# Performance work log

Hardware: AMD Instinct MI355X
Metric: run time of the kernel (lower is better)

Reference implementation:

```python
import jax, jax.numpy as jnp
import numpy as np

N_NODES = 50000


def _gcn_layer(x, edge_index, W, b, relu):
    """tf_geometric-style GCN: h = D^-1/2 (A+I) D^-1/2 (x @ W) + b, opt relu."""
    n = x.shape[0]
    h = x @ W  # [N, D_out] transform first (standard GCN)
    src, dst = edge_index[0], edge_index[1]
    sl = jnp.arange(n, dtype=src.dtype)
    src = jnp.concatenate([src, sl])  # add self-loops (renorm trick)
    dst = jnp.concatenate([dst, sl])
    deg = jax.ops.segment_sum(jnp.ones_like(dst, dtype=h.dtype), dst, num_segments=n)
    dinv = jax.lax.rsqrt(jnp.maximum(deg, 1e-12))
    norm = dinv[src] * dinv[dst]  # symmetric normalization per edge
    msg = h[src] * norm[:, None]  # [E+N, D_out] gather + scale
    out = jax.ops.segment_sum(msg, dst, num_segments=n) + b
    return jax.nn.relu(out) if relu else out


def setup_inputs() -> dict:
    key = jax.random.key(0)
    ks = jax.random.split(key, 12)
    F, E = 512, 800000
    d = {}
    d["x"] = jax.random.normal(ks[0], (N_NODES, F), dtype=jnp.float32)
    d["edge_index1"] = jax.random.randint(ks[1], (2, E), 0, N_NODES, dtype=jnp.int32)
    d["edge_index2"] = jax.random.randint(ks[2], (2, E), 0, N_NODES, dtype=jnp.int32)
    def glorot(k, shape):
        lim = np.sqrt(6.0 / (shape[0] + shape[1])).astype(np.float32)
        return jax.random.uniform(k, shape, jnp.float32, -lim, lim)
    d["W10"] = glorot(ks[3], (F, 256)); d["b10"] = jnp.zeros((256,), jnp.float32)
    d["W20"] = glorot(ks[4], (F, 64));  d["b20"] = jnp.zeros((64,), jnp.float32)
    d["W21"] = glorot(ks[5], (64, 256)); d["b21"] = jnp.zeros((256,), jnp.float32)
    d["Wfc"] = glorot(ks[6], (256, 16)); d["bfc"] = jnp.zeros((16,), jnp.float32)
    return d


def reference(x, edge_index1, edge_index2, W10, b10, W20, b20, W21, b21, Wfc, bfc):
    h1 = _gcn_layer(x, edge_index1, W10, b10, relu=True)   # GCN(256, relu)
    h2 = _gcn_layer(x, edge_index2, W20, b20, relu=False)  # GCN(64)
    h2 = _gcn_layer(h2, edge_index2, W21, b21, relu=True)  # GCN(256, relu)
    h = h1 + h2
    return h @ Wfc + bfc  # Dense(class_num)
```

## Files before the change

### kernel.cpp

```cpp
#include <hip/hip_runtime.h>
#include <hip/hip_bf16.h>
#include <cstdint>
#include <cstddef>

#define N_NODES 50000
#define FDIM 512
#define NBKT 391
#define CHUNK 8192
#define BCAP 4096

typedef __bf16 bf16_t;
typedef bf16_t bf16x8 __attribute__((ext_vector_type(8)));
typedef float f32x4 __attribute__((ext_vector_type(4)));

__device__ __forceinline__ unsigned short f2bf(float f) {
  union { float f; uint32_t u; } c; c.f = f;
  uint32_t u = c.u;
  uint32_t r = (u + 0x7fffu + ((u >> 16) & 1u)) >> 16;
  return (unsigned short)r;
}
__device__ __forceinline__ float bf2f(unsigned short u) {
  union { uint32_t i; float f; } c; c.i = (uint32_t)u << 16; return c.f;
}
__device__ __forceinline__ float4 ld_bf4(const unsigned short* p) {
  ushort4 u = *(const ushort4*)p;
  float4 r; r.x = bf2f(u.x); r.y = bf2f(u.y); r.z = bf2f(u.z); r.w = bf2f(u.w);
  return r;
}
__device__ __forceinline__ void async16(const void* g, void* l) {
  __builtin_amdgcn_global_load_lds((const __attribute__((address_space(1))) void*)g,
                                   (__attribute__((address_space(3))) void*)l, 16, 0, 0);
}

__global__ __launch_bounds__(256) void binA(const int* __restrict__ d1, const int* __restrict__ d2,
                                            int* __restrict__ M1, int* __restrict__ M2,
                                            int E1, int E2, int nch1, int nch2) {
  const int g = blockIdx.y;
  const int* dst = g ? d2 : d1;
  int* M = g ? M2 : M1;
  const int E = g ? E2 : E1;
  const int nch = g ? nch2 : nch1;
  const int chunk = blockIdx.x;
  if (chunk >= nch) return;
  __shared__ int cnt[NBKT];
  for (int j = threadIdx.x; j < NBKT; j += 256) cnt[j] = 0;
  __syncthreads();
  const int base = chunk * CHUNK;
#pragma unroll 4
  for (int i = 0; i < CHUNK / 256; i++) {
    int e = base + i * 256 + threadIdx.x;
    if (e < E) atomicAdd(&cnt[dst[e] >> 7], 1);
  }
  __syncthreads();
  for (int j = threadIdx.x; j < NBKT; j += 256) M[chunk * NBKT + j] = cnt[j];
}

__global__ __launch_bounds__(512) void bin_offsets(int* __restrict__ M1, int* __restrict__ M2,
                                                   int* __restrict__ bases,
                                                   int nch1, int nch2, int E1, int E2) {
  const int g = blockIdx.x;
  int* M = g ? M2 : M1;
  const int nch = g ? nch2 : nch1;
  int* base = bases + g * (NBKT + 1);
  const int E = g ? E2 : E1;
  const int t = threadIdx.x;
  __shared__ int tot[512];
  int running = 0;
  if (t < NBKT) {
    for (int b = 0; b < nch; b++) {
      int v = M[b * NBKT + t];
      M[b * NBKT + t] = running;
      running += v;
    }
  }
  tot[t] = (t < NBKT) ? running : 0;
  __syncthreads();
  for (int off = 1; off < 512; off <<= 1) {
    int u = (t >= off) ? tot[t - off] : 0;
    __syncthreads();
    tot[t] += u;
    __syncthreads();
  }
  int ex = (t == 0) ? 0 : tot[t - 1];
  if (t < NBKT) {
    base[t] = ex;
    for (int b = 0; b < nch; b++) M[b * NBKT + t] += ex;
  }
  if (t == NBKT) base[NBKT] = E;
}

__global__ __launch_bounds__(256) void binB(const int* __restrict__ s1, const int* __restrict__ d1,
                                            const int* __restrict__ M1, unsigned* __restrict__ eb1,
                                            int E1, int nch1,
                                            const int* __restrict__ s2, const int* __restrict__ d2,
                                            const int* __restrict__ M2, unsigned* __restrict__ eb2,
                                            int E2, int nch2) {
  const int g = blockIdx.y;
  const int* src = g ? s2 : s1;
  const int* dst = g ? d2 : d1;
  const int* M = g ? M2 : M1;
  unsigned* eb = g ? eb2 : eb1;
  const int E = g ? E2 : E1;
  const int nch = g ? nch2 : nch1;
  const int chunk = blockIdx.x;
  if (chunk >= nch) return;
  __shared__ int gbase[NBKT];
  __shared__ int cur[NBKT];
  for (int j = threadIdx.x; j < NBKT; j += 256) {
    gbase[j] = M[chunk * NBKT + j];
    cur[j] = 0;
  }
  __syncthreads();
  const int base = chunk * CHUNK;
#pragma unroll 4
  for (int i = 0; i < CHUNK / 256; i++) {
    int e = base + i * 256 + threadIdx.x;
    if (e < E) {
      int d = dst[e];
      int b = d >> 7;
      int pos = gbase[b] + atomicAdd(&cur[b], 1);
      eb[pos] = ((unsigned)d << 16) | (unsigned)src[e];
    }
  }
}

__global__ __launch_bounds__(256) void binC(const unsigned* __restrict__ eb1,
                                            const unsigned* __restrict__ eb2,
                                            const int* __restrict__ bases,
                                            int* __restrict__ rp1, float* __restrict__ dv1,
                                            int* __restrict__ cs1,
                                            int* __restrict__ rp2, float* __restrict__ dv2,
                                            int* __restrict__ cs2, int n) {
  const int g = blockIdx.y;
  const unsigned* eb = g ? eb2 : eb1;
  const int* base = bases + g * (NBKT + 1);
  int* rp = g ? rp2 : rp1;
  float* dv = g ? dv2 : dv1;
  int* cs = g ? cs2 : cs1;
  const int bkt = blockIdx.x;
  const int e0 = base[bkt], e1 = base[bkt + 1];
  const int cnt = e1 - e0;
  const int node0 = bkt << 7;
  const int t = threadIdx.x;
  __shared__ unsigned stage[BCAP];
  __shared__ int sorted[BCAP];
  __shared__ int dcnt[128], dcur[128], dscan[128];
  if (t < 128) dcnt[t] = 0;
  __syncthreads();
  for (int i = t; i < cnt; i += 256) {
    unsigned pe = eb[e0 + i];
    stage[i] = pe;
    atomicAdd(&dcnt[(pe >> 16) & 127], 1);
  }
  __syncthreads();
  if (t < 128) dscan[t] = dcnt[t];
  __syncthreads();
  for (int off = 1; off < 128; off <<= 1) {
    int u = (t < 128 && t >= off) ? dscan[t - off] : 0;
    __syncthreads();
    if (t < 128) dscan[t] += u;
    __syncthreads();
  }
  if (t < 128) {
    int ex = dscan[t] - dcnt[t];
    dcur[t] = ex;
    int node = node0 + t;
    if (node < n) {
      rp[node] = e0 + ex;
      dv[node] = rsqrtf((float)dcnt[t] + 1.0f);
    }
  }
  __syncthreads();
  for (int i = t; i < cnt; i += 256) {
    unsigned pe = stage[i];
    int d = (pe >> 16) & 127;
    int pos = atomicAdd(&dcur[d], 1);
    sorted[pos] = (int)(pe & 0xFFFFu);
  }
  __syncthreads();
  for (int i = t; i < cnt; i += 256) cs[e0 + i] = sorted[i];
  if (bkt == NBKT - 1 && t == 0) rp[n] = base[NBKT];
}

__global__ void cvt_w(const float* __restrict__ W10, const float* __restrict__ W20,
                      const float* __restrict__ W21, unsigned short* __restrict__ WcatT,
                      unsigned short* __restrict__ W21T) {
  int j = blockIdx.x * 256 + threadIdx.x;
  const int T1 = 384 * 512;
  if (j < T1) {
    int n = j >> 9, k = j & 511;
    float v = (n < 256) ? W10[k * 256 + n] : ((n < 320) ? W20[k * 64 + (n - 256)] : 0.f);
    WcatT[j] = f2bf(v);
  } else {
    int j2 = j - T1;
    if (j2 < 256 * 64) {
      int n = j2 >> 6, k = j2 & 63;
      W21T[j2] = f2bf(W21[k * 256 + n]);
    }
  }
}

__global__ __launch_bounds__(256) void g1(const float* __restrict__ X,
                                          const unsigned short* __restrict__ B,
                                          unsigned short* __restrict__ o1,
                                          unsigned short* __restrict__ o2, int M) {
  __shared__ __attribute__((aligned(16))) unsigned short As[128 * 64];
  __shared__ __attribute__((aligned(16))) unsigned short Bs[128 * 64];
  const int tid = threadIdx.x;
  const int w = tid >> 6, lane = tid & 63;
  const int row0 = blockIdx.x * 128;
  const int n0 = blockIdx.y * 128;
  const int lr = lane >> 3, lc8 = (lane & 7) * 8;
  const int wm = w >> 1, wn = w & 1;
  const int mlane = lane & 15, q = lane >> 4;

  f32x4 acc[4][4];
#pragma unroll
  for (int mi = 0; mi < 4; mi++)
#pragma unroll
    for (int ni = 0; ni < 4; ni++) {
      f32x4 z = {0.f, 0.f, 0.f, 0.f};
      acc[mi][ni] = z;
    }

  for (int k0 = 0; k0 < 512; k0 += 64) {
    __syncthreads();
#pragma unroll
    for (int i = 0; i < 8; i++) {
      int j = i * 256 + tid;
      int r = j >> 4, c4 = j & 15;
      int gr = row0 + r; if (gr > M - 1) gr = M - 1;
      float4 v = *(const float4*)(X + (size_t)gr * 512 + k0 + c4 * 4);
      ushort4 o; o.x = f2bf(v.x); o.y = f2bf(v.y); o.z = f2bf(v.z); o.w = f2bf(v.w);
      *(ushort4*)&As[r * 64 + c4 * 4] = o;
    }
#pragma unroll
    for (int i = 0; i < 4; i++) {
      int n = i * 32 + w * 8 + lr;
      async16(B + (size_t)(n0 + n) * 512 + k0 + lc8, &Bs[(i * 32 + w * 8) * 64]);
    }
    __syncthreads();
#pragma unroll
    for (int kk = 0; kk < 2; kk++) {
      bf16x8 af[4], bfr[4];
#pragma unroll
      for (int mi = 0; mi < 4; mi++)
        af[mi] = *(const bf16x8*)&As[(wm * 64 + mi * 16 + mlane) * 64 + kk * 32 + q * 8];
#pragma unroll
      for (int ni = 0; ni < 4; ni++)
        bfr[ni] = *(const bf16x8*)&Bs[(wn * 64 + ni * 16 + mlane) * 64 + kk * 32 + q * 8];
#pragma unroll
      for (int mi = 0; mi < 4; mi++)
#pragma unroll
        for (int ni = 0; ni < 4; ni++)
          acc[mi][ni] = __builtin_amdgcn_mfma_f32_16x16x32_bf16(af[mi], bfr[ni], acc[mi][ni], 0, 0, 0);
    }
  }

#pragma unroll
  for (int mi = 0; mi < 4; mi++)
#pragma unroll
    for (int ni = 0; ni < 4; ni++) {
      int c = n0 + wn * 64 + ni * 16 + mlane;
#pragma unroll
      for (int rg = 0; rg < 4; rg++) {
        int r = row0 + wm * 64 + mi * 16 + q * 4 + rg;
        if (r < M) {
          float v = acc[mi][ni][rg];
          if (c < 256) o1[(size_t)r * 256 + c] = f2bf(v);
          else if (c < 320) o2[(size_t)r * 64 + (c - 256)] = f2bf(v);
        }
      }
    }
}

__global__ __launch_bounds__(256) void prop256(const unsigned short* __restrict__ H,
                                               const int* __restrict__ rp,
                                               const int* __restrict__ cs,
                                               const float* __restrict__ dinv,
                                               const float* __restrict__ bias,
                                               float* __restrict__ out, int n) {
  const int i = blockIdx.x * 4 + (threadIdx.x >> 6);
  const int l = threadIdx.x & 63;
  if (i >= n) return;
  const float di = dinv[i];
  float4 self = ld_bf4(H + (size_t)i * 256 + l * 4);
  float4 acc;
  acc.x = di * self.x; acc.y = di * self.y; acc.z = di * self.z; acc.w = di * self.w;
  const int e1 = rp[i + 1];
#pragma unroll 4
  for (int e = rp[i]; e < e1; e++) {
    int s = cs[e];
    float wgt = dinv[s];
    float4 rrow = ld_bf4(H + (size_t)s * 256 + l * 4);
    acc.x += wgt * rrow.x; acc.y += wgt * rrow.y; acc.z += wgt * rrow.z; acc.w += wgt * rrow.w;
  }
  float4 b = *(const float4*)(bias + l * 4);
  float4 o;
  o.x = fmaxf(di * acc.x + b.x, 0.f);
  o.y = fmaxf(di * acc.y + b.y, 0.f);
  o.z = fmaxf(di * acc.z + b.z, 0.f);
  o.w = fmaxf(di * acc.w + b.w, 0.f);
  *(float4*)(out + (size_t)i * 256 + l * 4) = o;
}

template <int BIAS>
__global__ __launch_bounds__(256) void prop64(const unsigned short* __restrict__ H,
                                              const int* __restrict__ rp,
                                              const int* __restrict__ cs,
                                              const float* __restrict__ dinv,
                                              const float* __restrict__ bias,
                                              unsigned short* __restrict__ out, int n) {
  const int i = blockIdx.x * 16 + (threadIdx.x >> 4);
  const int l = threadIdx.x & 15;
  if (i >= n) return;
  const float di = dinv[i];
  float4 self = ld_bf4(H + (size_t)i * 64 + l * 4);
  float4 acc;
  acc.x = di * self.x; acc.y = di * self.y; acc.z = di * self.z; acc.w = di * self.w;
  const int e1 = rp[i + 1];
#pragma unroll 4
  for (int e = rp[i]; e < e1; e++) {
    int s = cs[e];
    float wgt = dinv[s];
    float4 rrow = ld_bf4(H + (size_t)s * 64 + l * 4);
    acc.x += wgt * rrow.x; acc.y += wgt * rrow.y; acc.z += wgt * rrow.z; acc.w += wgt * rrow.w;
  }
  float4 o;
  o.x = di * acc.x; o.y = di * acc.y; o.z = di * acc.z; o.w = di * acc.w;
  if (BIAS) {
    float4 b = *(const float4*)(bias + l * 4);
    o.x += b.x; o.y += b.y; o.z += b.z; o.w += b.w;
  }
  ushort4 ob;
  ob.x = f2bf(o.x); ob.y = f2bf(o.y); ob.z = f2bf(o.z); ob.w = f2bf(o.w);
  *(ushort4*)(out + (size_t)i * 64 + l * 4) = ob;
}

__global__ __launch_bounds__(512) void gf(const unsigned short* __restrict__ A,
                                          const unsigned short* __restrict__ Bb,
                                          const float* __restrict__ h1,
                                          const float* __restrict__ b21,
                                          const float* __restrict__ Wfc,
                                          const float* __restrict__ bfc,
                                          float* __restrict__ out, int M) {
  __shared__ __attribute__((aligned(16))) float hsm[128 * 260];
  __shared__ __attribute__((aligned(16))) float wt[256 * 16];
  unsigned short* As = (unsigned short*)hsm;
  unsigned short* Bs = As + 128 * 64;
  const int tid = threadIdx.x;
  const int w = tid >> 6, lane = tid & 63;
  const int row0 = blockIdx.x * 128;
  const int wm = w >> 2, wn = w & 3;
  const int mlane = lane & 15, q = lane >> 4;

  for (int j = tid; j < 4096; j += 512) wt[j] = Wfc[j];
#pragma unroll
  for (int i = 0; i < 2; i++) {
    int gr = row0 + i * 64 + w * 8 + (lane >> 3);
    if (gr > M - 1) gr = M - 1;
    async16(A + (size_t)gr * 64 + (lane & 7) * 8, &As[(i * 64 + w * 8) * 64]);
  }
#pragma unroll
  for (int i = 0; i < 4; i++) {
    int n = i * 64 + w * 8 + (lane >> 3);
    async16(Bb + (size_t)n * 64 + (lane & 7) * 8, &Bs[(i * 64 + w * 8) * 64]);
  }
  __syncthreads();

  f32x4 acc[4][4];
#pragma unroll
  for (int mi = 0; mi < 4; mi++)
#pragma unroll
    for (int ni = 0; ni < 4; ni++) {
      f32x4 z = {0.f, 0.f, 0.f, 0.f};
      acc[mi][ni] = z;
    }
#pragma unroll
  for (int kk = 0; kk < 2; kk++) {
    bf16x8 af[4], bfr[4];
#pragma unroll
    for (int mi = 0; mi < 4; mi++)
      af[mi] = *(const bf16x8*)&As[(wm * 64 + mi * 16 + mlane) * 64 + kk * 32 + q * 8];
#pragma unroll
    for (int ni = 0; ni < 4; ni++)
      bfr[ni] = *(const bf16x8*)&Bs[(wn * 64 + ni * 16 + mlane) * 64 + kk * 32 + q * 8];
#pragma unroll
    for (int mi = 0; mi < 4; mi++)
#pragma unroll
      for (int ni = 0; ni < 4; ni++)
        acc[mi][ni] = __builtin_amdgcn_mfma_f32_16x16x32_bf16(af[mi], bfr[ni], acc[mi][ni], 0, 0, 0);
  }
  __syncthreads();

#pragma unroll
  for (int ni = 0; ni < 4; ni++) {
    int c = wn * 64 + ni * 16 + mlane;
    float bb = b21[c];
#pragma unroll
    for (int mi = 0; mi < 4; mi++)
#pragma unroll
      for (int rg = 0; rg < 4; rg++) {
        int rl = wm * 64 + mi * 16 + q * 4 + rg;
        int gr = row0 + rl;
        int grc = (gr < M) ? gr : (M - 1);
        float v = fmaxf(acc[mi][ni][rg] + bb, 0.f) + h1[(size_t)grc * 256 + c];
        hsm[rl * 260 + c] = v;
      }
  }
  __syncthreads();

  const int r = tid >> 2, j0 = (tid & 3) * 4;
  const int gr = row0 + r;
  if (gr < M) {
    float4 s = *(const float4*)(bfc + j0);
    const float* hrow = &hsm[r * 260];
#pragma unroll 8
    for (int c4 = 0; c4 < 64; c4++) {
      float4 h4 = *(const float4*)(hrow + c4 * 4);
      const float* wp = &wt[(c4 * 4) * 16 + j0];
      float4 a0 = *(const float4*)(wp);
      float4 a1 = *(const float4*)(wp + 16);
      float4 a2 = *(const float4*)(wp + 32);
      float4 a3 = *(const float4*)(wp + 48);
      s.x += h4.x * a0.x + h4.y * a1.x + h4.z * a2.x + h4.w * a3.x;
      s.y += h4.x * a0.y + h4.y * a1.y + h4.z * a2.y + h4.w * a3.y;
      s.z += h4.x * a0.z + h4.y * a1.z + h4.z * a2.z + h4.w * a3.z;
      s.w += h4.x * a0.w + h4.y * a1.w + h4.z * a2.w + h4.w * a3.w;
    }
    *(float4*)(out + (size_t)gr * 16 + j0) = s;
  }
}

extern "C" void kernel_launch(void* const* d_in, const int* in_sizes, int n_in,
                              void* d_out, int out_size, void* d_ws, size_t ws_size,
                              hipStream_t stream) {
  const float* X   = (const float*)d_in[0];
  const int*   ei1 = (const int*)d_in[1];
  const int*   ei2 = (const int*)d_in[2];
  const float* W10 = (const float*)d_in[3];
  const float* b10 = (const float*)d_in[4];
  const float* W20 = (const float*)d_in[5];
  const float* b20 = (const float*)d_in[6];
  const float* W21 = (const float*)d_in[7];
  const float* b21 = (const float*)d_in[8];
  const float* Wfc = (const float*)d_in[9];
  const float* bfc = (const float*)d_in[10];
  float* out = (float*)d_out;

  const int N = N_NODES;
  const int E1 = in_sizes[1] / 2, E2 = in_sizes[2] / 2;
  const int* src1 = ei1; const int* dst1 = ei1 + E1;
  const int* src2 = ei2; const int* dst2 = ei2 + E2;
  const int nch1 = (E1 + CHUNK - 1) / CHUNK, nch2 = (E2 + CHUNK - 1) / CHUNK;
  const int nchmax = (nch1 > nch2) ? nch1 : nch2;

  char* p = (char*)d_ws;
  auto alloc = [&](size_t b) { char* r = p; p += (b + 255) & ~(size_t)255; return (void*)r; };
  int* M1 = (int*)alloc((size_t)nch1 * NBKT * 4);
  int* M2 = (int*)alloc((size_t)nch2 * NBKT * 4);
  int* bases = (int*)alloc((size_t)2 * (NBKT + 1) * 4);
  unsigned* eb1 = (unsigned*)alloc((size_t)E1 * 4);
  unsigned* eb2 = (unsigned*)alloc((size_t)E2 * 4);
  int* rp1 = (int*)alloc((size_t)(N + 1) * 4);
  int* rp2 = (int*)alloc((size_t)(N + 1) * 4);
  float* dinv1 = (float*)alloc((size_t)N * 4);
  float* dinv2 = (float*)alloc((size_t)N * 4);
  int* csr1s = (int*)alloc((size_t)E1 * 4);
  int* csr2s = (int*)alloc((size_t)E2 * 4);
  unsigned short* WcatT = (unsigned short*)alloc(384 * 512 * 2);
  unsigned short* W21T  = (unsigned short*)alloc(256 * 64 * 2);
  unsigned short* Xh1b = (unsigned short*)alloc((size_t)N * 256 * 2);
  unsigned short* Xh2b = (unsigned short*)alloc((size_t)N * 64 * 2);
  unsigned short* h2b  = (unsigned short*)alloc((size_t)N * 64 * 2);
  unsigned short* q2b  = (unsigned short*)alloc((size_t)N * 64 * 2);
  float* h1 = (float*)alloc((size_t)N * 256 * 4);

  binA<<<dim3(nchmax, 2), 256, 0, stream>>>(dst1, dst2, M1, M2, E1, E2, nch1, nch2);
  bin_offsets<<<dim3(2), 512, 0, stream>>>(M1, M2, bases, nch1, nch2, E1, E2);
  binB<<<dim3(nchmax, 2), 256, 0, stream>>>(src1, dst1, M1, eb1, E1, nch1,
                                            src2, dst2, M2, eb2, E2, nch2);
  binC<<<dim3(NBKT, 2), 256, 0, stream>>>(eb1, eb2, bases, rp1, dinv1, csr1s,
                                          rp2, dinv2, csr2s, N);
  cvt_w<<<dim3((384 * 512 + 256 * 64 + 255) / 256), 256, 0, stream>>>(W10, W20, W21, WcatT, W21T);
  g1<<<dim3((N + 127) / 128, 3), 256, 0, stream>>>(X, WcatT, Xh1b, Xh2b, N);
  prop256<<<dim3((N + 3) / 4), 256, 0, stream>>>(Xh1b, rp1, csr1s, dinv1, b10, h1, N);
  prop64<1><<<dim3((N + 15) / 16), 256, 0, stream>>>(Xh2b, rp2, csr2s, dinv2, b20, h2b, N);
  prop64<0><<<dim3((N + 15) / 16), 256, 0, stream>>>(h2b, rp2, csr2s, dinv2, nullptr, q2b, N);
  gf<<<dim3((N + 127) / 128), 512, 0, stream>>>(q2b, W21T, h1, b21, Wfc, bfc, out, N);
}
```

Measured before the change: 429.3 us.

## Widen first GEMM N-tile to 192 and prefetch X into registers across k-steps

The X@Wcat GEMM now uses 128x192 tiles with a grid of 2 column blocks instead of 3. The fp32 X matrix is therefore read twice rather than three times. The next k-slice of X is prefetched into registers while the current slice is converted and computed, with explicit waitcnt and barrier scheduling. This cuts redundant global reads of X and hides load latency, at the cost of more accumulator registers (24 MFMA tiles) and more LDS, which may lower occupancy. It also adds unroll pragmas to the bin offset loops.

Measured after the change: 430.7 us. Within noise of the previous version (+0.3%).

```diff
diff --git a/kernel.cpp b/kernel.cpp
--- a/kernel.cpp
+++ b/kernel.cpp
@@ -67,6 +67,7 @@
   __shared__ int tot[512];
   int running = 0;
   if (t < NBKT) {
+#pragma unroll 4
     for (int b = 0; b < nch; b++) {
       int v = M[b * NBKT + t];
       M[b * NBKT + t] = running;
@@ -84,6 +85,7 @@
   int ex = (t == 0) ? 0 : tot[t - 1];
   if (t < NBKT) {
     base[t] = ex;
+#pragma unroll 4
     for (int b = 0; b < nch; b++) M[b * NBKT + t] += ex;
   }
   if (t == NBKT) base[NBKT] = E;
@@ -200,59 +202,84 @@
   }
 }
 
-__global__ __launch_bounds__(256) void g1(const float* __restrict__ X,
-                                          const unsigned short* __restrict__ B,
-                                          unsigned short* __restrict__ o1,
-                                          unsigned short* __restrict__ o2, int M) {
+__global__ __launch_bounds__(256) void g1w(const float* __restrict__ X,
+                                           const unsigned short* __restrict__ B,
+                                           unsigned short* __restrict__ o1,
+                                           unsigned short* __restrict__ o2, int M) {
   __shared__ __attribute__((aligned(16))) unsigned short As[128 * 64];
-  __shared__ __attribute__((aligned(16))) unsigned short Bs[128 * 64];
+  __shared__ __attribute__((aligned(16))) unsigned short Bs[192 * 64];
   const int tid = threadIdx.x;
   const int w = tid >> 6, lane = tid & 63;
   const int row0 = blockIdx.x * 128;
-  const int n0 = blockIdx.y * 128;
-  const int lr = lane >> 3, lc8 = (lane & 7) * 8;
+  const int n0 = blockIdx.y * 192;
   const int wm = w >> 1, wn = w & 1;
   const int mlane = lane & 15, q = lane >> 4;
 
-  f32x4 acc[4][4];
+  const int ar = tid >> 4;
+  const int ac4 = tid & 15;
+
+  f32x4 acc[4][6];
 #pragma unroll
   for (int mi = 0; mi < 4; mi++)
 #pragma unroll
-    for (int ni = 0; ni < 4; ni++) {
+    for (int ni = 0; ni < 6; ni++) {
       f32x4 z = {0.f, 0.f, 0.f, 0.f};
       acc[mi][ni] = z;
     }
 
+  float4 areg[8];
+#pragma unroll
+  for (int i = 0; i < 8; i++) {
+    int gr = row0 + i * 16 + ar; if (gr > M - 1) gr = M - 1;
+    areg[i] = *(const float4*)(X + (size_t)gr * 512 + ac4 * 4);
+  }
+
   for (int k0 = 0; k0 < 512; k0 += 64) {
     __syncthreads();
 #pragma unroll
     for (int i = 0; i < 8; i++) {
-      int j = i * 256 + tid;
-      int r = j >> 4, c4 = j & 15;
-      int gr = row0 + r; if (gr > M - 1) gr = M - 1;
-      float4 v = *(const float4*)(X + (size_t)gr * 512 + k0 + c4 * 4);
-      ushort4 o; o.x = f2bf(v.x); o.y = f2bf(v.y); o.z = f2bf(v.z); o.w = f2bf(v.w);
-      *(ushort4*)&As[r * 64 + c4 * 4] = o;
-    }
-#pragma unroll
-    for (int i = 0; i < 4; i++) {
-      int n = i * 32 + w * 8 + lr;
-      async16(B + (size_t)(n0 + n) * 512 + k0 + lc8, &Bs[(i * 32 + w * 8) * 64]);
-    }
-    __syncthreads();
+      ushort4 o;
+      o.x = f2bf(areg[i].x); o.y = f2bf(areg[i].y);
+      o.z = f2bf(areg[i].z); o.w = f2bf(areg[i].w);
+      *(ushort4*)&As[(i * 16 + ar) * 64 + ac4 * 4] = o;
+    }
+#pragma unroll
+    for (int i = 0; i < 6; i++) {
+      int idx = i * 256 + tid;
+      int rw = idx >> 3, c8 = idx & 7;
+      async16(B + (size_t)(n0 + rw) * 512 + k0 + c8 * 8, &Bs[rw * 64 + c8 * 8]);
+    }
+    __builtin_amdgcn_sched_barrier(0);
+    const bool lastk = (k0 == 448);
+    if (!lastk) {
+#pragma unroll
+      for (int i = 0; i < 8; i++) {
+        int gr = row0 + i * 16 + ar; if (gr > M - 1) gr = M - 1;
+        areg[i] = *(const float4*)(X + (size_t)gr * 512 + (k0 + 64) + ac4 * 4);
+      }
+    }
+    __builtin_amdgcn_sched_barrier(0);
+    if (!lastk) {
+      asm volatile("s_waitcnt vmcnt(8) lgkmcnt(0)" ::: "memory");
+    } else {
+      asm volatile("s_waitcnt vmcnt(0) lgkmcnt(0)" ::: "memory");
+    }
+    __builtin_amdgcn_sched_barrier(0);
+    __builtin_amdgcn_s_barrier();
+    __builtin_amdgcn_sched_barrier(0);
 #pragma unroll
     for (int kk = 0; kk < 2; kk++) {
-      bf16x8 af[4], bfr[4];
+      bf16x8 af[4], bfr[6];
 #pragma unroll
       for (int mi = 0; mi < 4; mi++)
         af[mi] = *(const bf16x8*)&As[(wm * 64 + mi * 16 + mlane) * 64 + kk * 32 + q * 8];
 #pragma unroll
-      for (int ni = 0; ni < 4; ni++)
-        bfr[ni] = *(const bf16x8*)&Bs[(wn * 64 + ni * 16 + mlane) * 64 + kk * 32 + q * 8];
+      for (int ni = 0; ni < 6; ni++)
+        bfr[ni] = *(const bf16x8*)&Bs[(wn * 96 + ni * 16 + mlane) * 64 + kk * 32 + q * 8];
 #pragma unroll
       for (int mi = 0; mi < 4; mi++)
 #pragma unroll
-        for (int ni = 0; ni < 4; ni++)
+        for (int ni = 0; ni < 6; ni++)
           acc[mi][ni] = __builtin_amdgcn_mfma_f32_16x16x32_bf16(af[mi], bfr[ni], acc[mi][ni], 0, 0, 0);
     }
   }
@@ -260,8 +287,8 @@
 #pragma unroll
   for (int mi = 0; mi < 4; mi++)
 #pragma unroll
-    for (int ni = 0; ni < 4; ni++) {
-      int c = n0 + wn * 64 + ni * 16 + mlane;
+    for (int ni = 0; ni < 6; ni++) {
+      int c = n0 + wn * 96 + ni * 16 + mlane;
 #pragma unroll
       for (int rg = 0; rg < 4; rg++) {
         int r = row0 + wm * 64 + mi * 16 + q * 4 + rg;
@@ -483,7 +510,7 @@
   binC<<<dim3(NBKT, 2), 256, 0, stream>>>(eb1, eb2, bases, rp1, dinv1, csr1s,
                                           rp2, dinv2, csr2s, N);
   cvt_w<<<dim3((384 * 512 + 256 * 64 + 255) / 256), 256, 0, stream>>>(W10, W20, W21, WcatT, W21T);
-  g1<<<dim3((N + 127) / 128, 3), 256, 0, stream>>>(X, WcatT, Xh1b, Xh2b, N);
+  g1w<<<dim3((N + 127) / 128, 2), 256, 0, stream>>>(X, WcatT, Xh1b, Xh2b, N);
   prop256<<<dim3((N + 3) / 4), 256, 0, stream>>>(Xh1b, rp1, csr1s, dinv1, b10, h1, N);
   prop64<1><<<dim3((N + 15) / 16), 256, 0, stream>>>(Xh2b, rp2, csr2s, dinv2, b20, h2b, N);
   prop64<0><<<dim3((N + 15) / 16), 256, 0, stream>>>(h2b, rp2, csr2s, dinv2, nullptr, q2b, N);
```

## Compute all output columns per block in first GEMM with swizzled LDS

Applied to the files above, without the earlier changes.

Replaces the 128x128 tile GEMM, which ran over a 3-wide column grid and re-read and re-converted each X tile three times, with a 64-row tile that computes all 320 useful output columns in one block. X is now read from global and converted to bf16 only once, and the padded 64 dummy columns are no longer computed. LDS tiles use an XOR swizzle to avoid bank conflicts, and global loads of X are issued before the B async copies to overlap latency. Unroll pragmas are also added to the bin offset loops. Each block now holds more accumulators (20 per wave), which raises register pressure, and B reuse per block drops.

New measurement: 392.4 us. 1.09x faster.

```diff
diff --git a/kernel.cpp b/kernel.cpp
--- a/kernel.cpp
+++ b/kernel.cpp
@@ -67,6 +67,7 @@
   __shared__ int tot[512];
   int running = 0;
   if (t < NBKT) {
+#pragma unroll 4
     for (int b = 0; b < nch; b++) {
       int v = M[b * NBKT + t];
       M[b * NBKT + t] = running;
@@ -84,6 +85,7 @@
   int ex = (t == 0) ? 0 : tot[t - 1];
   if (t < NBKT) {
     base[t] = ex;
+#pragma unroll 4
     for (int b = 0; b < nch; b++) M[b * NBKT + t] += ex;
   }
   if (t == NBKT) base[NBKT] = E;
@@ -200,59 +202,74 @@
   }
 }
 
-__global__ __launch_bounds__(256) void g1(const float* __restrict__ X,
+__global__ __launch_bounds__(256) void g2(const float* __restrict__ X,
                                           const unsigned short* __restrict__ B,
                                           unsigned short* __restrict__ o1,
                                           unsigned short* __restrict__ o2, int M) {
-  __shared__ __attribute__((aligned(16))) unsigned short As[128 * 64];
-  __shared__ __attribute__((aligned(16))) unsigned short Bs[128 * 64];
+  __shared__ __attribute__((aligned(16))) unsigned short As[64 * 64];
+  __shared__ __attribute__((aligned(16))) unsigned short Bs[320 * 64];
   const int tid = threadIdx.x;
   const int w = tid >> 6, lane = tid & 63;
-  const int row0 = blockIdx.x * 128;
-  const int n0 = blockIdx.y * 128;
-  const int lr = lane >> 3, lc8 = (lane & 7) * 8;
-  const int wm = w >> 1, wn = w & 1;
+  const int row0 = blockIdx.x * 64;
   const int mlane = lane & 15, q = lane >> 4;
 
-  f32x4 acc[4][4];
+  const int ar = tid >> 4;
+  const int ac4 = tid & 15;
+
+  f32x4 acc[4][5];
 #pragma unroll
   for (int mi = 0; mi < 4; mi++)
 #pragma unroll
-    for (int ni = 0; ni < 4; ni++) {
+    for (int ni = 0; ni < 5; ni++) {
       f32x4 z = {0.f, 0.f, 0.f, 0.f};
       acc[mi][ni] = z;
     }
 
   for (int k0 = 0; k0 < 512; k0 += 64) {
     __syncthreads();
-#pragma unroll
-    for (int i = 0; i < 8; i++) {
-      int j = i * 256 + tid;
-      int r = j >> 4, c4 = j & 15;
+    float4 areg[4];
+#pragma unroll
+    for (int i = 0; i < 4; i++) {
+      int r = i * 16 + ar;
       int gr = row0 + r; if (gr > M - 1) gr = M - 1;
-      float4 v = *(const float4*)(X + (size_t)gr * 512 + k0 + c4 * 4);
-      ushort4 o; o.x = f2bf(v.x); o.y = f2bf(v.y); o.z = f2bf(v.z); o.w = f2bf(v.w);
-      *(ushort4*)&As[r * 64 + c4 * 4] = o;
+      areg[i] = *(const float4*)(X + (size_t)gr * 512 + k0 + ac4 * 4);
+    }
+#pragma unroll
+    for (int i = 0; i < 10; i++) {
+      int idx = i * 256 + tid;
+      int rw = idx >> 3, c8 = idx & 7;
+      int sslot = c8 ^ (rw & 7);
+      async16(B + (size_t)rw * 512 + k0 + sslot * 8, &Bs[idx * 8]);
     }
 #pragma unroll
     for (int i = 0; i < 4; i++) {
-      int n = i * 32 + w * 8 + lr;
-      async16(B + (size_t)(n0 + n) * 512 + k0 + lc8, &Bs[(i * 32 + w * 8) * 64]);
+      int r = i * 16 + ar;
+      ushort4 o;
+      o.x = f2bf(areg[i].x); o.y = f2bf(areg[i].y);
+      o.z = f2bf(areg[i].z); o.w = f2bf(areg[i].w);
+      int slot = ((ac4 >> 1) ^ (r & 7));
+      *(ushort4*)&As[r * 64 + slot * 8 + (ac4 & 1) * 4] = o;
     }
     __syncthreads();
 #pragma unroll
     for (int kk = 0; kk < 2; kk++) {
-      bf16x8 af[4], bfr[4];
+      bf16x8 af[4], bfr[5];
+#pragma unroll
+      for (int mi = 0; mi < 4; mi++) {
+        int r = mi * 16 + mlane;
+        int slot = (kk * 4 + q) ^ (r & 7);
+        af[mi] = *(const bf16x8*)&As[r * 64 + slot * 8];
+      }
+#pragma unroll
+      for (int ni = 0; ni < 5; ni++) {
+        int r = w * 80 + ni * 16 + mlane;
+        int slot = (kk * 4 + q) ^ (r & 7);
+        bfr[ni] = *(const bf16x8*)&Bs[r * 64 + slot * 8];
+      }
 #pragma unroll
       for (int mi = 0; mi < 4; mi++)
-        af[mi] = *(const bf16x8*)&As[(wm * 64 + mi * 16 + mlane) * 64 + kk * 32 + q * 8];
-#pragma unroll
-      for (int ni = 0; ni < 4; ni++)
-        bfr[ni] = *(const bf16x8*)&Bs[(wn * 64 + ni * 16 + mlane) * 64 + kk * 32 + q * 8];
-#pragma unroll
-      for (int mi = 0; mi < 4; mi++)
-#pragma unroll
-        for (int ni = 0; ni < 4; ni++)
+#pragma unroll
+        for (int ni = 0; ni < 5; ni++)
           acc[mi][ni] = __builtin_amdgcn_mfma_f32_16x16x32_bf16(af[mi], bfr[ni], acc[mi][ni], 0, 0, 0);
     }
   }
@@ -260,15 +277,15 @@
 #pragma unroll
   for (int mi = 0; mi < 4; mi++)
 #pragma unroll
-    for (int ni = 0; ni < 4; ni++) {
-      int c = n0 + wn * 64 + ni * 16 + mlane;
+    for (int ni = 0; ni < 5; ni++) {
+      int c = w * 80 + ni * 16 + mlane;
 #pragma unroll
       for (int rg = 0; rg < 4; rg++) {
-        int r = row0 + wm * 64 + mi * 16 + q * 4 + rg;
+        int r = row0 + mi * 16 + q * 4 + rg;
         if (r < M) {
           float v = acc[mi][ni][rg];
           if (c < 256) o1[(size_t)r * 256 + c] = f2bf(v);
-          else if (c < 320) o2[(size_t)r * 64 + (c - 256)] = f2bf(v);
+          else o2[(size_t)r * 64 + (c - 256)] = f2bf(v);
         }
       }
     }
@@ -483,7 +500,7 @@
   binC<<<dim3(NBKT, 2), 256, 0, stream>>>(eb1, eb2, bases, rp1, dinv1, csr1s,
                                           rp2, dinv2, csr2s, N);
   cvt_w<<<dim3((384 * 512 + 256 * 64 + 255) / 256), 256, 0, stream>>>(W10, W20, W21, WcatT, W21T);
-  g1<<<dim3((N + 127) / 128, 3), 256, 0, stream>>>(X, WcatT, Xh1b, Xh2b, N);
+  g2<<<dim3((N + 63) / 64), 256, 0, stream>>>(X, WcatT, Xh1b, Xh2b, N);
   prop256<<<dim3((N + 3) / 4), 256, 0, stream>>>(Xh1b, rp1, csr1s, dinv1, b10, h1, N);
   prop64<1><<<dim3((N + 15) / 16), 256, 0, stream>>>(Xh2b, rp2, csr2s, dinv2, b20, h2b, N);
   prop64<0><<<dim3((N + 15) / 16), 256, 0, stream>>>(h2b, rp2, csr2s, dinv2, nullptr, q2b, N);
```
